# Kernel tuning notes

Hardware: AMD Instinct MI355X
Metric: run time of the kernel (lower is better)

The kernel has to match this reference:

```python
import jax, jax.numpy as jnp
import numpy as np

EPS = 1e-8
PHI = (1 + 5 ** 0.5) / 2
B, S, D, H, L, O = 8, 2048, 256, 512, 3, 1
NH = 4
HD = H // NH


def setup_inputs() -> dict:
    key = jax.random.key(0)
    ks = jax.random.split(key, 12)
    g = lambda k, shape, s=0.02: jax.random.normal(k, shape, dtype=jnp.float32) * s
    # Fibonacci modular spiral embedding (fixed, requires_grad=False in torch)
    idx = jnp.arange(D, dtype=jnp.float32)
    r = (PHI * idx) % 1.0
    th = 2 * jnp.pi * r
    phase_emb = jnp.stack([r * jnp.cos(th), r * jnp.sin(th)], axis=1)  # [D,2]
    return dict(
        x=jax.random.normal(ks[0], (B, S, D), dtype=jnp.float32),
        proj_w=g(ks[1], (D, D), 0.06), proj_b=jnp.zeros((D,), jnp.float32),
        phase_emb=phase_emb,
        hebb_w=g(ks[2], (H, 2), 0.5),
        attn_in_w=g(ks[3], (L, 3 * H, H)), attn_in_b=jnp.zeros((L, 3 * H), jnp.float32),
        attn_out_w=g(ks[4], (L, H, H)), attn_out_b=jnp.zeros((L, H), jnp.float32),
        ff1_w=g(ks[5], (L, 4 * H, H)), ff1_b=jnp.zeros((L, 4 * H), jnp.float32),
        ff2_w=g(ks[6], (L, H, 4 * H)), ff2_b=jnp.zeros((L, H), jnp.float32),
        ln1_w=jnp.ones((L, H), jnp.float32), ln1_b=jnp.zeros((L, H), jnp.float32),
        ln2_w=jnp.ones((L, H), jnp.float32), ln2_b=jnp.zeros((L, H), jnp.float32),
        normA_w=jnp.ones((H,), jnp.float32), normA_b=jnp.zeros((H,), jnp.float32),
        normB_w=jnp.ones((H // 2,), jnp.float32), normB_b=jnp.zeros((H // 2,), jnp.float32),
        p1_w=g(ks[7], (H // 2, H), 0.04), p1_b=jnp.zeros((H // 2,), jnp.float32),
        p2_w=g(ks[8], (O, H // 2), 0.06), p2_b=jnp.zeros((O,), jnp.float32),
    )


def _ln(x, w, b, eps=1e-5):
    m = x.mean(-1, keepdims=True)
    v = ((x - m) ** 2).mean(-1, keepdims=True)
    return (x - m) * jax.lax.rsqrt(v + eps) * w + b


def _diffuse(psi, mask, dt, steps):
    # Norm-preserving RK2 integration of d(psi)/dt = mask@psi - psi
    def force(state):
        return jnp.einsum('bij,bjd->bid', mask, state) - state

    def step(p, _):
        r = jnp.linalg.norm(p, axis=-1, keepdims=True)
        k1 = force(p)
        ps = p + dt * k1
        ps = ps * (r / (jnp.linalg.norm(ps, axis=-1, keepdims=True) + EPS))
        k2 = force(ps)
        pn = p + 0.5 * dt * (k1 + k2)
        pn = pn * (r / (jnp.linalg.norm(pn, axis=-1, keepdims=True) + EPS))
        return pn, None

    psi, _ = jax.lax.scan(step, psi, None, length=steps)
    return psi


def _forward(x, proj_w, proj_b, phase_emb, hebb_w, attn_in_w, attn_in_b,
             attn_out_w, attn_out_b, ff1_w, ff1_b, ff2_w, ff2_b,
             ln1_w, ln1_b, ln2_w, ln2_b, normA_w, normA_b, normB_w, normB_b,
             p1_w, p1_b, p2_w, p2_b):
    b, s, _ = x.shape
    # PhaseHebbianEmbedder: project then map to 2D phase coords, unit-normalize
    xp = x @ proj_w.T + proj_b                               # [B,S,D]
    pc = jnp.einsum('bsd,dt->bst', xp, phase_emb)            # [B,S,2]
    psi = pc / (jnp.linalg.norm(pc, axis=-1, keepdims=True) + EPS)
    mask = jnp.broadcast_to(jnp.eye(s, dtype=x.dtype), (b, s, s))  # [B,S,S]
    psi = _diffuse(psi, mask, 0.1, 3)
    psi = _diffuse(psi, mask, 0.05, 4)
    A = jnp.einsum('bsd,btd->bst', psi, psi)                 # [B,S,S]
    final_psi = psi[:, -1]                                   # [B,2]
    h = (final_psi @ hebb_w.T)[:, None, :]                   # [B,1,H]
    for l in range(attn_in_w.shape[0]):
        qkv = h @ attn_in_w[l].T + attn_in_b[l]
        q, k, v = jnp.split(qkv, 3, axis=-1)
        hd = lambda t: t.reshape(b, -1, NH, HD).transpose(0, 2, 1, 3)
        q, k, v = hd(q), hd(k), hd(v)
        sc = jnp.einsum('bhqd,bhkd->bhqk', q, k) / jnp.sqrt(jnp.float32(HD))
        att = jax.nn.softmax(sc, axis=-1)
        o = jnp.einsum('bhqk,bhkd->bhqd', att, v).transpose(0, 2, 1, 3).reshape(b, -1, H)
        o = o @ attn_out_w[l].T + attn_out_b[l]
        h = _ln(h + o, ln1_w[l], ln1_b[l])
        ff = jax.nn.silu(h @ ff1_w[l].T + ff1_b[l]) @ ff2_w[l].T + ff2_b[l]
        h = _ln(h + ff, ln2_w[l], ln2_b[l])
    h = _ln(h[:, 0, :], normA_w, normA_b)
    p = jax.nn.silu(h @ p1_w.T + p1_b)
    p = _ln(p, normB_w, normB_b)
    preds = p @ p2_w.T + p2_b                                # [B,O]
    return preds, A, mask, psi


def reference(x, proj_w, proj_b, phase_emb, hebb_w, attn_in_w, attn_in_b,
              attn_out_w, attn_out_b, ff1_w, ff1_b, ff2_w, ff2_b,
              ln1_w, ln1_b, ln2_w, ln2_b, normA_w, normA_b, normB_w, normB_b,
              p1_w, p1_b, p2_w, p2_b):
    return _forward(x, proj_w, proj_b, phase_emb, hebb_w, attn_in_w, attn_in_b,
                    attn_out_w, attn_out_b, ff1_w, ff1_b, ff2_w, ff2_b,
                    ln1_w, ln1_b, ln2_w, ln2_b, normA_w, normA_b,
                    normB_w, normB_b, p1_w, p1_b, p2_w, p2_b)
```

## Files before the change

kernel.cpp:

```cpp
#include <hip/hip_runtime.h>
#include <hip/hip_bf16.h>

#define BB 8
#define SS 2048
#define DD 256
#define HH 512
#define LL 3
#define NROWS (BB * SS)
#define PSIBLK 1024
#define WCBN 192

typedef float floatx4 __attribute__((ext_vector_type(4)));

__device__ __forceinline__ void amask_row(const float* __restrict__ psi,
                                          float* __restrict__ A, float* __restrict__ M,
                                          int blk)
{
    int tid = threadIdx.x;
    int b = blk >> 11, i = blk & (SS - 1);
    float2 pi = *reinterpret_cast<const float2*>(psi + (size_t)blk * 2);
    #pragma unroll
    for (int c = 0; c < 2; ++c) {
        int j0 = c * 1024 + tid * 4;
        const float4* pr = reinterpret_cast<const float4*>(psi + ((size_t)b * SS + j0) * 2);
        float4 q0 = pr[0], q1 = pr[1];
        floatx4 o;
        o.x = pi.x * q0.x + pi.y * q0.y;
        o.y = pi.x * q0.z + pi.y * q0.w;
        o.z = pi.x * q1.x + pi.y * q1.y;
        o.w = pi.x * q1.z + pi.y * q1.w;
        size_t rb = (size_t)blk * SS + j0;
        __builtin_nontemporal_store(o, reinterpret_cast<floatx4*>(A + rb));
        floatx4 m;
        m.x = (i == j0    ) ? 1.f : 0.f;
        m.y = (i == j0 + 1) ? 1.f : 0.f;
        m.z = (i == j0 + 2) ? 1.f : 0.f;
        m.w = (i == j0 + 3) ? 1.f : 0.f;
        __builtin_nontemporal_store(m, reinterpret_cast<floatx4*>(M + rb));
    }
}

__global__ void psiM_kernel(const float* __restrict__ x,
                            const float* __restrict__ pw, const float* __restrict__ pb,
                            const float* __restrict__ pe, const float* __restrict__ hebb,
                            const float* __restrict__ ai_w, const float* __restrict__ ai_b,
                            const float* __restrict__ ao_w, const float* __restrict__ ao_b,
                            float* __restrict__ psi, float* __restrict__ h0,
                            float* __restrict__ Wc, float* __restrict__ bc)
{
    __shared__ __align__(16) float sB[8 * HH];
    const int tid = threadIdx.x;
    const int bid = blockIdx.x;

    if (bid >= PSIBLK) {
        int wcb = bid - PSIBLK;
        int l = wcb >> 6;
        int j0 = (wcb & 63) * 8;
        const float* WoB = ao_w + (size_t)l * HH * HH;
        for (int idx = tid; idx < 8 * HH; idx += 256) {
            int r = idx >> 9, m = idx & 511;
            sB[idx] = WoB[(size_t)(j0 + r) * HH + m];
        }
        __syncthreads();
        const float* WvB = ai_w + ((size_t)l * 3 * HH + 2 * HH) * HH;
        int k0 = tid, k1 = tid + 256;
        float acc0[8] = {0,0,0,0,0,0,0,0};
        float acc1[8] = {0,0,0,0,0,0,0,0};
        for (int m = 0; m < HH; ++m) {
            float w0 = WvB[(size_t)m * HH + k0];
            float w1 = WvB[(size_t)m * HH + k1];
            #pragma unroll
            for (int r = 0; r < 8; ++r) {
                float wo = sB[r * HH + m];
                acc0[r] = fmaf(wo, w0, acc0[r]);
                acc1[r] = fmaf(wo, w1, acc1[r]);
            }
        }
        #pragma unroll
        for (int r = 0; r < 8; ++r) {
            Wc[((size_t)l * HH + j0 + r) * HH + k0] = acc0[r];
            Wc[((size_t)l * HH + j0 + r) * HH + k1] = acc1[r];
        }
        if (tid < 8) {
            const float* bvB = ai_b + l * 3 * HH + 2 * HH;
            float s = ao_b[l * HH + j0 + tid];
            for (int m = 0; m < HH; ++m) s += sB[tid * HH + m] * bvB[m];
            bc[l * HH + j0 + tid] = s;
        }
        return;
    }

    {
        float a0 = 0.f, a1 = 0.f;
        for (int d = 0; d < DD; ++d) {
            float w = pw[d * DD + tid];
            a0 += w * pe[2 * d];
            a1 += w * pe[2 * d + 1];
        }
        sB[2 * tid] = a0;
        sB[2 * tid + 1] = a1;
        if (tid < 64) {
            float c0 = 0.f, c1 = 0.f;
            for (int d = tid; d < DD; d += 64) {
                c0 += pb[d] * pe[2 * d];
                c1 += pb[d] * pe[2 * d + 1];
            }
            #pragma unroll
            for (int dd = 32; dd; dd >>= 1) {
                c0 += __shfl_xor(c0, dd);
                c1 += __shfl_xor(c1, dd);
            }
            if (tid == 0) { sB[512] = c0; sB[513] = c1; }
        }
    }
    __syncthreads();

    int wave = tid >> 6, lane = tid & 63;
    const float4* sM4 = reinterpret_cast<const float4*>(sB);
    float4 mA = sM4[lane * 2];
    float4 mB = sM4[lane * 2 + 1];
    float c0 = sB[512], c1 = sB[513];
    int base = bid * 16 + wave * 4;
    #pragma unroll
    for (int it = 0; it < 4; ++it) {
        int rid = base + it;
        float4 v = *reinterpret_cast<const float4*>(x + (size_t)rid * DD + lane * 4);
        float a0 = v.x * mA.x + v.y * mA.z + v.z * mB.x + v.w * mB.z;
        float a1 = v.x * mA.y + v.y * mA.w + v.z * mB.y + v.w * mB.w;
        #pragma unroll
        for (int d = 32; d; d >>= 1) {
            a0 += __shfl_xor(a0, d);
            a1 += __shfl_xor(a1, d);
        }
        a0 += c0;
        a1 += c1;
        float n = sqrtf(a0 * a0 + a1 * a1);
        float scale = 1.f / (n + 1e-8f);
        float r = n * scale;
        #pragma unroll
        for (int i7 = 0; i7 < 7; ++i7) {
            float f = r / (r + 1e-8f);
            scale *= f;
            r *= f;
        }
        float px = a0 * scale, py = a1 * scale;
        if (lane == 0) {
            float2 pv;
            pv.x = px;
            pv.y = py;
            *reinterpret_cast<float2*>(psi + (size_t)rid * 2) = pv;
        }
        if ((rid & (SS - 1)) == SS - 1) {
            int b = rid >> 11;
            for (int j = lane; j < HH; j += 64)
                h0[(size_t)b * HH + j] = px * hebb[2 * j] + py * hebb[2 * j + 1];
        }
    }
}

__global__ void head_mm(const float* __restrict__ X, int K,
                        const float* __restrict__ xlnw, const float* __restrict__ xlnb,
                        const float* __restrict__ xln2w, const float* __restrict__ xln2b,
                        const float* __restrict__ W, const float* __restrict__ bias,
                        const float* __restrict__ res,
                        const float* __restrict__ reslnw, const float* __restrict__ reslnb,
                        float* __restrict__ out, int J, int G, int act,
                        const float* __restrict__ psi,
                        float* __restrict__ Ao, float* __restrict__ Mo,
                        int mmBlocks, int arow0)
{
    const int bid = blockIdx.x;
    if (bid >= mmBlocks) {
        int r = arow0 + (bid - mmBlocks);
        if (r < NROWS) amask_row(psi, Ao, Mo, r);
        return;
    }

    extern __shared__ float sX[];
    __shared__ float s_m[8], s_r[8], s_rm[8], s_rr[8];
    const int tid = threadIdx.x;
    const int row = tid >> 5, lane = tid & 31;
    const bool doLN = (xlnw != nullptr);
    const bool doRLN = (res != nullptr) && (reslnw != nullptr);

    if (doLN) {
        float s = 0.f, ss = 0.f;
        for (int k = lane; k < K; k += 32) {
            float v = X[row * K + k];
            s += v; ss += v * v;
        }
        for (int d = 16; d; d >>= 1) { s += __shfl_down(s, d); ss += __shfl_down(ss, d); }
        if (lane == 0) {
            float m = s / K;
            s_m[row] = m;
            s_r[row] = rsqrtf(ss / K - m * m + 1e-5f);
        }
    }
    if (doRLN) {
        float s = 0.f, ss = 0.f;
        for (int k = lane; k < J; k += 32) {
            float v = res[row * J + k];
            s += v; ss += v * v;
        }
        for (int d = 16; d; d >>= 1) { s += __shfl_down(s, d); ss += __shfl_down(ss, d); }
        if (lane == 0) {
            float m = s / J;
            s_rm[row] = m;
            s_rr[row] = rsqrtf(ss / J - m * m + 1e-5f);
        }
    }
    __syncthreads();

    if (doLN) {
        for (int idx = tid; idx < 8 * K; idx += 256) {
            int b = idx / K, k = idx - b * K;
            sX[idx] = (X[idx] - s_m[b]) * s_r[b] * xlnw[k] + xlnb[k];
        }
        __syncthreads();
        if (xln2w) {
            float s = 0.f, ss = 0.f;
            for (int k = lane; k < K; k += 32) {
                float v = sX[row * K + k];
                s += v; ss += v * v;
            }
            for (int d = 16; d; d >>= 1) { s += __shfl_down(s, d); ss += __shfl_down(ss, d); }
            if (lane == 0) {
                float m = s / K;
                s_m[row] = m;
                s_r[row] = rsqrtf(ss / K - m * m + 1e-5f);
            }
            __syncthreads();
            for (int idx = tid; idx < 8 * K; idx += 256) {
                int b = idx / K, k = idx - b * K;
                sX[idx] = (sX[idx] - s_m[b]) * s_r[b] * xln2w[k] + xln2b[k];
            }
            __syncthreads();
        }
    }

    const float* __restrict__ Xp = doLN ? (const float*)sX : X;
    const int g = tid & (G - 1);
    const int jj = tid / G;
    const int j = bid * (256 / G) + jj;

    float acc[8] = {0.f, 0.f, 0.f, 0.f, 0.f, 0.f, 0.f, 0.f};
    if (j < J) {
        const float4* W4 = reinterpret_cast<const float4*>(W + (size_t)j * K);
        const int K4 = K >> 2;
        for (int i4 = g; i4 < K4; i4 += G) {
            float4 w4 = W4[i4];
            int k = i4 << 2;
            #pragma unroll
            for (int b = 0; b < 8; ++b) {
                float4 xv = *reinterpret_cast<const float4*>(Xp + b * K + k);
                acc[b] = fmaf(w4.x, xv.x, acc[b]);
                acc[b] = fmaf(w4.y, xv.y, acc[b]);
                acc[b] = fmaf(w4.z, xv.z, acc[b]);
                acc[b] = fmaf(w4.w, xv.w, acc[b]);
            }
        }
    }
    for (int d = G >> 1; d; d >>= 1) {
        #pragma unroll
        for (int b = 0; b < 8; ++b) acc[b] += __shfl_down(acc[b], d);
    }
    if (g == 0 && j < J) {
        float bs = bias ? bias[j] : 0.f;
        #pragma unroll
        for (int b = 0; b < 8; ++b) {
            float v = acc[b] + bs;
            if (act) v = v / (1.f + expf(-v));
            if (res) {
                float rv = res[(size_t)b * J + j];
                if (reslnw) rv = (rv - s_rm[b]) * s_rr[b] * reslnw[j] + reslnb[j];
                v += rv;
            }
            out[(size_t)b * J + j] = v;
        }
    }
}

extern "C" void kernel_launch(void* const* d_in, const int* in_sizes, int n_in,
                              void* d_out, int out_size, void* d_ws, size_t ws_size,
                              hipStream_t stream)
{
    const float* x      = (const float*)d_in[0];
    const float* proj_w = (const float*)d_in[1];
    const float* proj_b = (const float*)d_in[2];
    const float* pe     = (const float*)d_in[3];
    const float* hebb   = (const float*)d_in[4];
    const float* ai_w   = (const float*)d_in[5];
    const float* ai_b   = (const float*)d_in[6];
    const float* ao_w   = (const float*)d_in[7];
    const float* ao_b   = (const float*)d_in[8];
    const float* f1_w   = (const float*)d_in[9];
    const float* f1_b   = (const float*)d_in[10];
    const float* f2_w   = (const float*)d_in[11];
    const float* f2_b   = (const float*)d_in[12];
    const float* ln1w   = (const float*)d_in[13];
    const float* ln1b   = (const float*)d_in[14];
    const float* ln2w   = (const float*)d_in[15];
    const float* ln2b   = (const float*)d_in[16];
    const float* nAw    = (const float*)d_in[17];
    const float* nAb    = (const float*)d_in[18];
    const float* nBw    = (const float*)d_in[19];
    const float* nBb    = (const float*)d_in[20];
    const float* p1w    = (const float*)d_in[21];
    const float* p1b    = (const float*)d_in[22];
    const float* p2w    = (const float*)d_in[23];
    const float* p2b    = (const float*)d_in[24];

    float* out   = (float*)d_out;
    float* preds = out;
    float* A     = out + 8;
    float* Mask  = out + 8 + (size_t)BB * SS * SS;
    float* Psi   = out + 8 + (size_t)2 * BB * SS * SS;

    float* Wc = A + (size_t)15000 * SS;
    float* bc = Wc + 3 * HH * HH;

    float* ws = (float*)d_ws;
    float* T  = ws + 640;
    float* T1 = ws + 8832;
    float* F  = ws + 12928;
    float* P  = ws + 29312;

    psiM_kernel<<<PSIBLK + WCBN, 256, 0, stream>>>(
        x, proj_w, proj_b, pe, hebb, ai_w, ai_b, ao_w, ao_b, Psi, T, Wc, bc);

    int ci = 0, arow = 0;
    auto nextq = [&]() { int q = (ci < 10) ? 1490 : (NROWS - 1490 * 10); ++ci; return q; };

    for (int l = 0; l < LL; ++l) {
        const float* pxw = l ? ln2w + (l - 1) * HH : nullptr;
        const float* pxb = l ? ln2b + (l - 1) * HH : nullptr;
        int q;
        q = nextq();
        head_mm<<<64 + q, 256, (pxw ? 8 * HH * 4 : 0), stream>>>(
            T, HH, pxw, pxb, nullptr, nullptr,
            Wc + (size_t)l * HH * HH, bc + l * HH,
            T, pxw, pxb, T1, HH, 32, 0,
            Psi, A, Mask, 64, arow);
        arow += q;
        q = nextq();
        head_mm<<<128 + q, 256, 8 * HH * 4, stream>>>(
            T1, HH, ln1w + l * HH, ln1b + l * HH, nullptr, nullptr,
            f1_w + (size_t)l * 4 * HH * HH, f1_b + l * 4 * HH,
            nullptr, nullptr, nullptr, F, 4 * HH, 16, 1,
            Psi, A, Mask, 128, arow);
        arow += q;
        q = nextq();
        head_mm<<<128 + q, 256, 0, stream>>>(
            F, 4 * HH, nullptr, nullptr, nullptr, nullptr,
            f2_w + (size_t)l * HH * 4 * HH, f2_b + l * HH,
            T1, ln1w + l * HH, ln1b + l * HH, T, HH, 64, 0,
            Psi, A, Mask, 128, arow);
        arow += q;
    }
    {
        int q = nextq();
        head_mm<<<32 + q, 256, 8 * HH * 4, stream>>>(
            T, HH, ln2w + 2 * HH, ln2b + 2 * HH, nAw, nAb,
            p1w, p1b, nullptr, nullptr, nullptr, P, HH / 2, 32, 1,
            Psi, A, Mask, 32, arow);
        arow += q;
    }
    {
        int q = nextq();
        head_mm<<<1 + q, 256, 8 * (HH / 2) * 4, stream>>>(
            P, HH / 2, nBw, nBb, nullptr, nullptr,
            p2w, p2b, nullptr, nullptr, nullptr, preds, 1, 32, 0,
            Psi, A, Mask, 1, arow);
        arow += q;
    }
}
```

Baseline: 236.3 us.

## Split psi projection precompute, fuse head tail into one kernel, rebalance mask rows

Moves the proj_w·phase_emb reduction into a small one-block kernel so each of the 1024 psi blocks no longer recomputes the 256x256 contraction. It also unrolls the Wc weight-combination loop and parallelises the bias reduction across warps. The final two head launches become a single tail kernel that chains the LayerNorms, p1, SiLU and p2. A/mask row writing is spread evenly over 9 launches plus the tail. This removes redundant per-block work and one launch, at the cost of an extra tiny serial kernel at the start.

After: 292.6 us. +23.8%, slower.

```diff
diff --git a/kernel.cpp b/kernel.cpp
--- a/kernel.cpp
+++ b/kernel.cpp
@@ -7,7 +7,7 @@
 #define HH 512
 #define LL 3
 #define NROWS (BB * SS)
-#define PSIBLK 1024
+#define PSIB 1024
 #define WCBN 192
 
 typedef float floatx4 __attribute__((ext_vector_type(4)));
@@ -40,40 +40,82 @@
     }
 }
 
-__global__ void psiM_kernel(const float* __restrict__ x,
-                            const float* __restrict__ pw, const float* __restrict__ pb,
-                            const float* __restrict__ pe, const float* __restrict__ hebb,
-                            const float* __restrict__ ai_w, const float* __restrict__ ai_b,
-                            const float* __restrict__ ao_w, const float* __restrict__ ao_b,
-                            float* __restrict__ psi, float* __restrict__ h0,
-                            float* __restrict__ Wc, float* __restrict__ bc)
-{
-    __shared__ __align__(16) float sB[8 * HH];
+__global__ void compute_M(const float* __restrict__ pw, const float* __restrict__ pb,
+                          const float* __restrict__ pe, float* __restrict__ Mc)
+{
+    __shared__ float s0[4][256], s1[4][256];
+    int tid = threadIdx.x;
+    int k = tid & 255;
+    int sub = tid >> 8;
+    float a0 = 0.f, a1 = 0.f;
+    #pragma unroll 8
+    for (int d = sub * 64; d < sub * 64 + 64; ++d) {
+        float w = pw[d * DD + k];
+        a0 += w * pe[2 * d];
+        a1 += w * pe[2 * d + 1];
+    }
+    s0[sub][k] = a0;
+    s1[sub][k] = a1;
+    __syncthreads();
+    if (tid < 256) {
+        Mc[2 * tid]     = s0[0][tid] + s0[1][tid] + s0[2][tid] + s0[3][tid];
+        Mc[2 * tid + 1] = s1[0][tid] + s1[1][tid] + s1[2][tid] + s1[3][tid];
+    }
+    if (tid < 64) {
+        float c0 = 0.f, c1 = 0.f;
+        for (int d = tid; d < DD; d += 64) {
+            c0 += pb[d] * pe[2 * d];
+            c1 += pb[d] * pe[2 * d + 1];
+        }
+        #pragma unroll
+        for (int dd = 32; dd; dd >>= 1) {
+            c0 += __shfl_xor(c0, dd);
+            c1 += __shfl_xor(c1, dd);
+        }
+        if (tid == 0) { Mc[512] = c0; Mc[513] = c1; }
+    }
+}
+
+__global__ void psi_wc_kernel(const float* __restrict__ x, const float* __restrict__ Mc,
+                              const float* __restrict__ hebb,
+                              const float* __restrict__ ai_w, const float* __restrict__ ai_b,
+                              const float* __restrict__ ao_w, const float* __restrict__ ao_b,
+                              float* __restrict__ psi, float* __restrict__ T,
+                              float* __restrict__ Wc, float* __restrict__ bc)
+{
+    __shared__ __align__(16) float sW[8 * HH];
     const int tid = threadIdx.x;
     const int bid = blockIdx.x;
 
-    if (bid >= PSIBLK) {
-        int wcb = bid - PSIBLK;
+    if (bid >= PSIB) {
+        int wcb = bid - PSIB;
         int l = wcb >> 6;
         int j0 = (wcb & 63) * 8;
         const float* WoB = ao_w + (size_t)l * HH * HH;
         for (int idx = tid; idx < 8 * HH; idx += 256) {
             int r = idx >> 9, m = idx & 511;
-            sB[idx] = WoB[(size_t)(j0 + r) * HH + m];
+            sW[idx] = WoB[(size_t)(j0 + r) * HH + m];
         }
         __syncthreads();
         const float* WvB = ai_w + ((size_t)l * 3 * HH + 2 * HH) * HH;
         int k0 = tid, k1 = tid + 256;
         float acc0[8] = {0,0,0,0,0,0,0,0};
         float acc1[8] = {0,0,0,0,0,0,0,0};
-        for (int m = 0; m < HH; ++m) {
-            float w0 = WvB[(size_t)m * HH + k0];
-            float w1 = WvB[(size_t)m * HH + k1];
+        for (int m = 0; m < HH; m += 8) {
+            float av[8], bv8[8];
             #pragma unroll
-            for (int r = 0; r < 8; ++r) {
-                float wo = sB[r * HH + m];
-                acc0[r] = fmaf(wo, w0, acc0[r]);
-                acc1[r] = fmaf(wo, w1, acc1[r]);
+            for (int u = 0; u < 8; ++u) {
+                av[u]  = WvB[(size_t)(m + u) * HH + k0];
+                bv8[u] = WvB[(size_t)(m + u) * HH + k1];
+            }
+            #pragma unroll
+            for (int u = 0; u < 8; ++u) {
+                #pragma unroll
+                for (int r = 0; r < 8; ++r) {
+                    float wo = sW[r * HH + m + u];
+                    acc0[r] = fmaf(wo, av[u], acc0[r]);
+                    acc1[r] = fmaf(wo, bv8[u], acc1[r]);
+                }
             }
         }
         #pragma unroll
@@ -81,45 +123,23 @@
             Wc[((size_t)l * HH + j0 + r) * HH + k0] = acc0[r];
             Wc[((size_t)l * HH + j0 + r) * HH + k1] = acc1[r];
         }
-        if (tid < 8) {
+        {
+            int r = tid >> 5, lane = tid & 31;
             const float* bvB = ai_b + l * 3 * HH + 2 * HH;
-            float s = ao_b[l * HH + j0 + tid];
-            for (int m = 0; m < HH; ++m) s += sB[tid * HH + m] * bvB[m];
-            bc[l * HH + j0 + tid] = s;
+            float s = 0.f;
+            for (int m = lane; m < HH; m += 32) s += sW[r * HH + m] * bvB[m];
+            #pragma unroll
+            for (int d = 16; d; d >>= 1) s += __shfl_down(s, d);
+            if (lane == 0) bc[l * HH + j0 + r] = ao_b[l * HH + j0 + r] + s;
         }
         return;
     }
 
-    {
-        float a0 = 0.f, a1 = 0.f;
-        for (int d = 0; d < DD; ++d) {
-            float w = pw[d * DD + tid];
-            a0 += w * pe[2 * d];
-            a1 += w * pe[2 * d + 1];
-        }
-        sB[2 * tid] = a0;
-        sB[2 * tid + 1] = a1;
-        if (tid < 64) {
-            float c0 = 0.f, c1 = 0.f;
-            for (int d = tid; d < DD; d += 64) {
-                c0 += pb[d] * pe[2 * d];
-                c1 += pb[d] * pe[2 * d + 1];
-            }
-            #pragma unroll
-            for (int dd = 32; dd; dd >>= 1) {
-                c0 += __shfl_xor(c0, dd);
-                c1 += __shfl_xor(c1, dd);
-            }
-            if (tid == 0) { sB[512] = c0; sB[513] = c1; }
-        }
-    }
-    __syncthreads();
-
     int wave = tid >> 6, lane = tid & 63;
-    const float4* sM4 = reinterpret_cast<const float4*>(sB);
-    float4 mA = sM4[lane * 2];
-    float4 mB = sM4[lane * 2 + 1];
-    float c0 = sB[512], c1 = sB[513];
+    const float4* Mc4 = reinterpret_cast<const float4*>(Mc);
+    float4 mA = Mc4[lane * 2];
+    float4 mB = Mc4[lane * 2 + 1];
+    float c0 = Mc[512], c1 = Mc[513];
     int base = bid * 16 + wave * 4;
     #pragma unroll
     for (int it = 0; it < 4; ++it) {
@@ -153,14 +173,13 @@
         if ((rid & (SS - 1)) == SS - 1) {
             int b = rid >> 11;
             for (int j = lane; j < HH; j += 64)
-                h0[(size_t)b * HH + j] = px * hebb[2 * j] + py * hebb[2 * j + 1];
+                T[(size_t)b * HH + j] = px * hebb[2 * j] + py * hebb[2 * j + 1];
         }
     }
 }
 
 __global__ void head_mm(const float* __restrict__ X, int K,
                         const float* __restrict__ xlnw, const float* __restrict__ xlnb,
-                        const float* __restrict__ xln2w, const float* __restrict__ xln2b,
                         const float* __restrict__ W, const float* __restrict__ bias,
                         const float* __restrict__ res,
                         const float* __restrict__ reslnw, const float* __restrict__ reslnb,
@@ -217,25 +236,6 @@
             sX[idx] = (X[idx] - s_m[b]) * s_r[b] * xlnw[k] + xlnb[k];
         }
         __syncthreads();
-        if (xln2w) {
-            float s = 0.f, ss = 0.f;
-            for (int k = lane; k < K; k += 32) {
-                float v = sX[row * K + k];
-                s += v; ss += v * v;
-            }
-            for (int d = 16; d; d >>= 1) { s += __shfl_down(s, d); ss += __shfl_down(ss, d); }
-            if (lane == 0) {
-                float m = s / K;
-                s_m[row] = m;
-                s_r[row] = rsqrtf(ss / K - m * m + 1e-5f);
-            }
-            __syncthreads();
-            for (int idx = tid; idx < 8 * K; idx += 256) {
-                int b = idx / K, k = idx - b * K;
-                sX[idx] = (sX[idx] - s_m[b]) * s_r[b] * xln2w[k] + xln2b[k];
-            }
-            __syncthreads();
-        }
     }
 
     const float* __restrict__ Xp = doLN ? (const float*)sX : X;
@@ -277,6 +277,94 @@
             }
             out[(size_t)b * J + j] = v;
         }
+    }
+}
+
+__device__ __forceinline__ void ln8(const float* in, float* out, int N, int sh,
+                                    const float* __restrict__ w,
+                                    const float* __restrict__ bvec,
+                                    float* s_m, float* s_r, int tid)
+{
+    int row = tid >> 5, lane = tid & 31;
+    float s = 0.f, ss = 0.f;
+    for (int k = lane; k < N; k += 32) {
+        float v = in[(row << sh) + k];
+        s += v; ss += v * v;
+    }
+    #pragma unroll
+    for (int d = 16; d; d >>= 1) { s += __shfl_down(s, d); ss += __shfl_down(ss, d); }
+    if (lane == 0) {
+        float m = s / N;
+        s_m[row] = m;
+        s_r[row] = rsqrtf(ss / N - m * m + 1e-5f);
+    }
+    __syncthreads();
+    for (int idx = tid; idx < (N << 3); idx += 256) {
+        int b = idx >> sh, k = idx & (N - 1);
+        out[idx] = (in[idx] - s_m[b]) * s_r[b] * w[k] + bvec[k];
+    }
+    __syncthreads();
+}
+
+__global__ void tail_kernel(const float* __restrict__ T,
+                            const float* __restrict__ ln2w, const float* __restrict__ ln2b,
+                            const float* __restrict__ nAw, const float* __restrict__ nAb,
+                            const float* __restrict__ nBw, const float* __restrict__ nBb,
+                            const float* __restrict__ p1w, const float* __restrict__ p1b,
+                            const float* __restrict__ p2w, const float* __restrict__ p2b,
+                            float* __restrict__ preds,
+                            const float* __restrict__ psi,
+                            float* __restrict__ Ao, float* __restrict__ Mo, int arow0)
+{
+    const int bid = blockIdx.x;
+    const int tid = threadIdx.x;
+    if (bid >= 1) {
+        int r = arow0 + (bid - 1);
+        if (r < NROWS) amask_row(psi, Ao, Mo, r);
+        return;
+    }
+    __shared__ __align__(16) float sT[8 * HH];
+    __shared__ __align__(16) float sX[8 * HH];
+    __shared__ __align__(16) float sS[8 * 256];
+    __shared__ float s_m[8], s_r[8];
+    const float4* sX4 = reinterpret_cast<const float4*>(sX);
+
+    for (int idx = tid; idx < 4096; idx += 256) sT[idx] = T[idx];
+    __syncthreads();
+    ln8(sT, sX, HH, 9, ln2w + 2 * HH, ln2b + 2 * HH, s_m, s_r, tid);
+    ln8(sX, sX, HH, 9, nAw, nAb, s_m, s_r, tid);
+    {
+        int j = tid;
+        float acc[8] = {0,0,0,0,0,0,0,0};
+        const float4* W4 = reinterpret_cast<const float4*>(p1w + (size_t)j * HH);
+        for (int i4 = 0; i4 < 128; ++i4) {
+            float4 w = W4[i4];
+            #pragma unroll
+            for (int b = 0; b < 8; ++b) {
+                float4 xv = sX4[b * 128 + i4];
+                acc[b] = fmaf(w.x, xv.x, acc[b]);
+                acc[b] = fmaf(w.y, xv.y, acc[b]);
+                acc[b] = fmaf(w.z, xv.z, acc[b]);
+                acc[b] = fmaf(w.w, xv.w, acc[b]);
+            }
+        }
+        float bp = p1b[j];
+        #pragma unroll
+        for (int b = 0; b < 8; ++b) {
+            float v = acc[b] + bp;
+            v = v / (1.f + expf(-v));
+            sS[b * 256 + j] = v;
+        }
+    }
+    __syncthreads();
+    ln8(sS, sS, 256, 8, nBw, nBb, s_m, s_r, tid);
+    {
+        int b = tid >> 5, k = tid & 31;
+        float s = 0.f;
+        for (int kk = k; kk < 256; kk += 32) s += sS[b * 256 + kk] * p2w[kk];
+        #pragma unroll
+        for (int d = 16; d; d >>= 1) s += __shfl_down(s, d);
+        if (k == 0) preds[b] = s + p2b[0];
     }
 }
 
@@ -320,57 +408,43 @@
     float* bc = Wc + 3 * HH * HH;
 
     float* ws = (float*)d_ws;
+    float* Mc = ws;
     float* T  = ws + 640;
     float* T1 = ws + 8832;
     float* F  = ws + 12928;
-    float* P  = ws + 29312;
-
-    psiM_kernel<<<PSIBLK + WCBN, 256, 0, stream>>>(
-        x, proj_w, proj_b, pe, hebb, ai_w, ai_b, ao_w, ao_b, Psi, T, Wc, bc);
-
-    int ci = 0, arow = 0;
-    auto nextq = [&]() { int q = (ci < 10) ? 1490 : (NROWS - 1490 * 10); ++ci; return q; };
-
+
+    compute_M<<<1, 1024, 0, stream>>>(proj_w, proj_b, pe, Mc);
+    psi_wc_kernel<<<PSIB + WCBN, 256, 0, stream>>>(
+        x, Mc, hebb, ai_w, ai_b, ao_w, ao_b, Psi, T, Wc, bc);
+
+    int arow = 0;
+    const int QROW = 1639;
     for (int l = 0; l < LL; ++l) {
         const float* pxw = l ? ln2w + (l - 1) * HH : nullptr;
         const float* pxb = l ? ln2b + (l - 1) * HH : nullptr;
-        int q;
-        q = nextq();
-        head_mm<<<64 + q, 256, (pxw ? 8 * HH * 4 : 0), stream>>>(
-            T, HH, pxw, pxb, nullptr, nullptr,
+        head_mm<<<64 + QROW, 256, (pxw ? 8 * HH * 4 : 0), stream>>>(
+            T, HH, pxw, pxb,
             Wc + (size_t)l * HH * HH, bc + l * HH,
             T, pxw, pxb, T1, HH, 32, 0,
             Psi, A, Mask, 64, arow);
-        arow += q;
-        q = nextq();
-        head_mm<<<128 + q, 256, 8 * HH * 4, stream>>>(
-            T1, HH, ln1w + l * HH, ln1b + l * HH, nullptr, nullptr,
+        arow += QROW;
+        head_mm<<<128 + QROW, 256, 8 * HH * 4, stream>>>(
+            T1, HH, ln1w + l * HH, ln1b + l * HH,
             f1_w + (size_t)l * 4 * HH * HH, f1_b + l * 4 * HH,
             nullptr, nullptr, nullptr, F, 4 * HH, 16, 1,
             Psi, A, Mask, 128, arow);
-        arow += q;
-        q = nextq();
-        head_mm<<<128 + q, 256, 0, stream>>>(
-            F, 4 * HH, nullptr, nullptr, nullptr, nullptr,
+        arow += QROW;
+        head_mm<<<128 + QROW, 256, 0, stream>>>(
+            F, 4 * HH, nullptr, nullptr,
             f2_w + (size_t)l * HH * 4 * HH, f2_b + l * HH,
             T1, ln1w + l * HH, ln1b + l * HH, T, HH, 64, 0,
             Psi, A, Mask, 128, arow);
-        arow += q;
+        arow += QROW;
     }
     {
-        int q = nextq();
-        head_mm<<<32 + q, 256, 8 * HH * 4, stream>>>(
-            T, HH, ln2w + 2 * HH, ln2b + 2 * HH, nAw, nAb,
-            p1w, p1b, nullptr, nullptr, nullptr, P, HH / 2, 32, 1,
-            Psi, A, Mask, 32, arow);
-        arow += q;
-    }
-    {
-        int q = nextq();
-        head_mm<<<1 + q, 256, 8 * (HH / 2) * 4, stream>>>(
-            P, HH / 2, nBw, nBb, nullptr, nullptr,
-            p2w, p2b, nullptr, nullptr, nullptr, preds, 1, 32, 0,
-            Psi, A, Mask, 1, arow);
-        arow += q;
-    }
-}
+        int qrem = NROWS - arow;
+        tail_kernel<<<1 + qrem, 256, 0, stream>>>(
+            T, ln2w, ln2b, nAw, nAb, nBw, nBb, p1w, p1b, p2w, p2b,
+            preds, Psi, A, Mask, arow);
+    }
+}
```
